# Optimization experiments

Hardware: AMD Instinct MI355X
Metric: run time of the kernel (lower is better)

The kernel has to match this reference:

```python
import jax, jax.numpy as jnp
import numpy as np

B, T1, S = 32, 129, 256
E, H, K, V, VOCAB = 512, 1024, 128, 128, 8000


def _lstm_cell(x, h, c, W_ih, W_hh, b):
    # PyTorch LSTMCell gate order: i, f, g, o
    gates = x @ W_ih.T + h @ W_hh.T + b  # [B, 4H]
    i, f, g, o = jnp.split(gates, 4, axis=-1)
    c_new = jax.nn.sigmoid(f) * c + jax.nn.sigmoid(i) * jnp.tanh(g)
    h_new = jax.nn.sigmoid(o) * jnp.tanh(c_new)
    return h_new, c_new


def setup_inputs() -> dict:
    key = jax.random.key(0)
    ks = jax.random.split(key, 16)
    w = lambda k, shp: (jax.random.normal(k, shp, dtype=jnp.float32) * 0.02)
    return {
        "decoder_inputs": jax.random.randint(ks[0], (B, T1), 0, VOCAB),
        "inputs_lens": jax.random.randint(ks[1], (B,), 0, T1 - 1),
        "encoder_hidden": jax.random.normal(ks[2], (B, H), dtype=jnp.float32),
        "encoder_keys": jax.random.normal(ks[3], (B, S, K), dtype=jnp.float32),
        "encoder_values": jax.random.normal(ks[4], (B, S, V), dtype=jnp.float32),
        "embedding": w(ks[5], (VOCAB, E)),
        "W_ih1": w(ks[6], (4 * H, E + V)),
        "W_hh1": w(ks[7], (4 * H, H)),
        "b1": jnp.zeros((4 * H,), dtype=jnp.float32),
        "W_ih2": w(ks[8], (4 * H, H)),
        "W_hh2": w(ks[9], (4 * H, H)),
        "b2": jnp.zeros((4 * H,), dtype=jnp.float32),
        "W_q": w(ks[10], (K, H)),
        "b_q": jnp.zeros((K,), dtype=jnp.float32),
        "W_out": w(ks[11], (VOCAB, H + V)),
        "b_out": jnp.zeros((VOCAB,), dtype=jnp.float32),
    }


def reference(decoder_inputs, inputs_lens, encoder_hidden, encoder_keys,
              encoder_values, embedding, W_ih1, W_hh1, b1, W_ih2, W_hh2, b2,
              W_q, b_q, W_out, b_out):
    T = decoder_inputs.shape[1] - 1  # max_len = inputs.size(1) - 1
    # Teacher-forced embeddings, gathered once: [T, B, E]
    emb = jnp.swapaxes(embedding[decoder_inputs[:, :T]], 0, 1)

    h1 = h2 = encoder_hidden
    c1 = c2 = jnp.zeros_like(encoder_hidden)
    context0 = jnp.zeros((encoder_hidden.shape[0], encoder_values.shape[-1]),
                         dtype=encoder_hidden.dtype)

    def step(carry, emb_t):
        h1, c1, h2, c2, context = carry
        x = jnp.concatenate([emb_t, context], axis=1)  # [B, E+V]
        h1, c1 = _lstm_cell(x, h1, c1, W_ih1, W_hh1, b1)
        h2, c2 = _lstm_cell(h1, h2, c2, W_ih2, W_hh2, b2)
        # Attention over encoder keys/values
        q = h2 @ W_q.T + b_q                               # [B, K]
        energy = jnp.einsum('bsk,bk->bs', encoder_keys, q)  # [B, S]
        attn = jax.nn.softmax(energy, axis=-1)
        context = jnp.einsum('bs,bsv->bv', attn, encoder_values)  # [B, V]
        logits = jnp.concatenate([h2, context], axis=1) @ W_out.T + b_out
        return (h1, c1, h2, c2, context), logits

    _, logits = jax.lax.scan(step, (h1, c1, h2, c2, context0), emb)
    return jnp.swapaxes(logits, 0, 1)  # [B, T, VOCAB]
```

## Files before the change

kernel.cpp:

```cpp
#include <hip/hip_runtime.h>
#include <hip/hip_bf16.h>
#include <cstddef>

#define BB    32
#define T1    129
#define TT    128
#define SS    256
#define EE    512
#define HH    1024
#define KK    128
#define VV    128
#define VOC   8000
#define VOCP  8064
#define K1    1664
#define K2    2048
#define KLOG  1152
#define NF1   13
#define NF2   16
#define NBLK  256
#define NATT  32

typedef __bf16 bf16x8 __attribute__((ext_vector_type(8)));
typedef float  f32x4  __attribute__((ext_vector_type(4)));

#define MFMA(a,b,c) __builtin_amdgcn_mfma_f32_16x16x32_bf16((a),(b),(c),0,0,0)

#define CLOAD(dst, p) asm volatile("global_load_dwordx4 %0, %1, off sc0 sc1" : "=v"(dst) : "v"(p))

__device__ __forceinline__ int coh_load_i32(const int* p) {
    int r;
    asm volatile("global_load_dword %0, %1, off sc0 sc1\n\ts_waitcnt vmcnt(0)"
                 : "=v"(r) : "v"(p) : "memory");
    return r;
}
__device__ __forceinline__ void cstore_u16(__hip_bfloat16* p, __hip_bfloat16 v) {
    union { __hip_bfloat16 h; unsigned short u; } cv; cv.h = v;
    unsigned int val = cv.u;
    asm volatile("global_store_short %0, %1, off sc0 sc1" :: "v"(p), "v"(val) : "memory");
}
__device__ __forceinline__ void cstore_f32(float* p, float v) {
    asm volatile("global_store_dword %0, %1, off sc0 sc1" :: "v"(p), "v"(v) : "memory");
}

union bf8u { __hip_bfloat16 h[8]; bf16x8 v; };

__device__ __forceinline__ bf16x8 cvt8(float4 a, float4 b) {
    bf8u u;
    u.h[0] = __float2bfloat16(a.x); u.h[1] = __float2bfloat16(a.y);
    u.h[2] = __float2bfloat16(a.z); u.h[3] = __float2bfloat16(a.w);
    u.h[4] = __float2bfloat16(b.x); u.h[5] = __float2bfloat16(b.y);
    u.h[6] = __float2bfloat16(b.z); u.h[7] = __float2bfloat16(b.w);
    return u.v;
}

template<int SBASE, int NS>
__device__ __forceinline__ void coh_mfma(const __hip_bfloat16* rA, const __hip_bfloat16* rB,
                                         int wv, const bf16x8* wf, f32x4& a0, f32x4& a1)
{
    bf16x8 fA[NS], fB[NS];
    #pragma unroll
    for (int s = 0; s < NS; ++s) {
        int k0 = (wv + 4 * (SBASE + s)) * 32;
        CLOAD(fA[s], rA + k0);
        CLOAD(fB[s], rB + k0);
    }
    asm volatile("s_waitcnt vmcnt(0)" ::: "memory");
    __builtin_amdgcn_sched_barrier(0);
    #pragma unroll
    for (int s = 0; s < NS; ++s) {
        a0 = MFMA(fA[s], wf[SBASE + s], a0);
        a1 = MFMA(fB[s], wf[SBASE + s], a1);
    }
}

__device__ __forceinline__ void grid_barrier(int* bar, int bid, int& gen)
{
    asm volatile("s_waitcnt vmcnt(0)" ::: "memory");
    __syncthreads();
    if (threadIdx.x == 0) {
        int target = gen + 1;
        int prev = __hip_atomic_fetch_add(&bar[(bid >> 5) * 32], 1,
                                          __ATOMIC_RELAXED, __HIP_MEMORY_SCOPE_AGENT);
        if (((prev + 1) & 31) == 0) {
            int pr = __hip_atomic_fetch_add(&bar[320], 1,
                                            __ATOMIC_RELAXED, __HIP_MEMORY_SCOPE_AGENT);
            if (((pr + 1) & 7) == 0)
                __hip_atomic_fetch_add(&bar[384], 1,
                                       __ATOMIC_RELAXED, __HIP_MEMORY_SCOPE_AGENT);
        }
        while (coh_load_i32(&bar[384]) < target)
            __builtin_amdgcn_s_sleep(4);
        gen = target;
    }
    __syncthreads();
}

__global__ void pack_wout(const float* __restrict__ W, __hip_bfloat16* __restrict__ Wp)
{
    int v = blockIdx.y;
    int k = blockIdx.x * 256 + threadIdx.x;
    if (k >= KLOG) return;
    float w = (v < VOC) ? W[(size_t)v * KLOG + k] : 0.f;
    Wp[(size_t)v * KLOG + k] = __float2bfloat16(w);
}

__global__ void init_state(const float* __restrict__ enc,
                           __hip_bfloat16* __restrict__ A1,
                           __hip_bfloat16* __restrict__ A2,
                           int* __restrict__ bar)
{
    int i = blockIdx.x * 256 + threadIdx.x;
    if (i < 1024) bar[i] = 0;
    if (i >= BB * HH) return;
    int b = i >> 10, j = i & 1023;
    float e = enc[i];
    __hip_bfloat16 eb = __float2bfloat16(e);
    A2[(size_t)b * K2 + HH + j]        = eb;
    A1[(size_t)b * K1 + (EE + VV) + j] = eb;
    if (j < VV) A1[(size_t)b * K1 + EE + j] = __float2bfloat16(0.f);
}

__global__ void gather_emb(const int* __restrict__ tok, const float* __restrict__ emb,
                           __hip_bfloat16* __restrict__ A1)
{
    int bid = blockIdx.x;
    int t = bid >> 5, b = bid & 31;
    int id = tok[b * T1 + t];
    const float* er = emb + (size_t)id * EE;
    __hip_bfloat16* dst = A1 + (size_t)t * BB * K1 + (size_t)b * K1;
    for (int k = threadIdx.x; k < EE; k += 256)
        dst[k] = __float2bfloat16(er[k]);
}

__global__ __launch_bounds__(256) void decoder_persistent(
    const float* __restrict__ Wih1, const float* __restrict__ Whh1, const float* __restrict__ b1v,
    const float* __restrict__ Wih2, const float* __restrict__ Whh2, const float* __restrict__ b2v,
    const float* __restrict__ Wq,   const float* __restrict__ bq,
    const float* __restrict__ keys, const float* __restrict__ vals,
    __hip_bfloat16* A1, __hip_bfloat16* A2,
    __hip_bfloat16* Alog, float* h2f, int* bar)
{
    const int bid = blockIdx.x;
    const int tid = threadIdx.x;
    const int wv  = tid >> 6;
    const int l   = tid & 63;
    const int l15 = l & 15, l4 = l >> 4;
    const int n0  = bid * 16;

    __shared__ float G[4][32][17];
    __shared__ float hs[HH];
    __shared__ float qs[KK];
    __shared__ float es[SS];
    __shared__ float red[256];

    bf16x8 w1f[NF1], w2f[NF2];
    {
        const int col  = n0 + l15;
        const int orow = (col & 3) * HH + (col >> 2);
        #pragma unroll
        for (int s = 0; s < NF1; ++s) {
            int k0 = (wv + 4 * s) * 32 + l4 * 8;
            const float* src = (k0 < EE + VV) ? (Wih1 + (size_t)orow * (EE + VV) + k0)
                                              : (Whh1 + (size_t)orow * HH + (k0 - (EE + VV)));
            w1f[s] = cvt8(*(const float4*)src, *(const float4*)(src + 4));
        }
        #pragma unroll
        for (int s = 0; s < NF2; ++s) {
            int k0 = (wv + 4 * s) * 32 + l4 * 8;
            const float* src = (k0 < HH) ? (Wih2 + (size_t)orow * HH + k0)
                                         : (Whh2 + (size_t)orow * HH + (k0 - HH));
            w2f[s] = cvt8(*(const float4*)src, *(const float4*)(src + 4));
        }
    }

    float c1r = 0.f, c2r = 0.f;
    float gb1[4], gb2[4];
    {
        int jl = (tid >> 5) & 3;
        int j  = (n0 >> 2) + jl;
        #pragma unroll
        for (int g = 0; g < 4; ++g) { gb1[g] = b1v[g * HH + j]; gb2[g] = b2v[g * HH + j]; }
    }

    int gen = 0;
    const size_t a1s = (size_t)BB * K1;
    const size_t a2s = (size_t)BB * K2;

    #pragma unroll 1
    for (int t = 0; t < TT; ++t) {
        const __hip_bfloat16* A1t = A1 + (size_t)t * a1s;
        __hip_bfloat16* A1n   = A1 + (size_t)(t + 1) * a1s;
        __hip_bfloat16* A2c   = A2 + (size_t)(t & 1) * a2s;
        __hip_bfloat16* A2n   = A2 + (size_t)((t + 1) & 1) * a2s;
        __hip_bfloat16* AlogT = Alog + (size_t)t * BB * KLOG;

        {
            f32x4 acc0 = {0.f,0.f,0.f,0.f}, acc1 = {0.f,0.f,0.f,0.f};
            const __hip_bfloat16* rA = A1t + (size_t)l15 * K1 + l4 * 8;
            const __hip_bfloat16* rB = rA + (size_t)16 * K1;
            #pragma unroll
            for (int s = 0; s < 4; ++s) {
                int k0 = (wv + 4 * s) * 32;
                bf16x8 a0 = *(const bf16x8*)(rA + k0);
                bf16x8 a1 = *(const bf16x8*)(rB + k0);
                acc0 = MFMA(a0, w1f[s], acc0);
                acc1 = MFMA(a1, w1f[s], acc1);
            }
            coh_mfma<4, 9>(rA, rB, wv, w1f, acc0, acc1);

            #pragma unroll
            for (int r = 0; r < 4; ++r) {
                G[wv][l4 * 4 + r][l15]      = acc0[r];
                G[wv][16 + l4 * 4 + r][l15] = acc1[r];
            }
        }
        __syncthreads();
        if (tid < 128) {
            int b = tid & 31, jl = tid >> 5;
            float g0 = G[0][b][4*jl+0] + G[1][b][4*jl+0] + G[2][b][4*jl+0] + G[3][b][4*jl+0] + gb1[0];
            float g1 = G[0][b][4*jl+1] + G[1][b][4*jl+1] + G[2][b][4*jl+1] + G[3][b][4*jl+1] + gb1[1];
            float g2 = G[0][b][4*jl+2] + G[1][b][4*jl+2] + G[2][b][4*jl+2] + G[3][b][4*jl+2] + gb1[2];
            float g3 = G[0][b][4*jl+3] + G[1][b][4*jl+3] + G[2][b][4*jl+3] + G[3][b][4*jl+3] + gb1[3];
            float si = 1.f / (1.f + __expf(-g0));
            float sf = 1.f / (1.f + __expf(-g1));
            float so = 1.f / (1.f + __expf(-g3));
            c1r = sf * c1r + si * tanhf(g2);
            float h = so * tanhf(c1r);
            int j = (n0 >> 2) + jl;
            __hip_bfloat16 hb = __float2bfloat16(h);
            cstore_u16(&A2c[(size_t)b * K2 + j], hb);
            if (t + 1 < TT) cstore_u16(&A1n[(size_t)b * K1 + EE + VV + j], hb);
        }
        grid_barrier(bar, bid, gen);

        {
            f32x4 acc0 = {0.f,0.f,0.f,0.f}, acc1 = {0.f,0.f,0.f,0.f};
            const __hip_bfloat16* rA = A2c + (size_t)l15 * K2 + l4 * 8;
            const __hip_bfloat16* rB = rA + (size_t)16 * K2;
            coh_mfma<0, 8>(rA, rB, wv, w2f, acc0, acc1);
            coh_mfma<8, 8>(rA, rB, wv, w2f, acc0, acc1);
            #pragma unroll
            for (int r = 0; r < 4; ++r) {
                G[wv][l4 * 4 + r][l15]      = acc0[r];
                G[wv][16 + l4 * 4 + r][l15] = acc1[r];
            }
        }
        __syncthreads();
        if (tid < 128) {
            int b = tid & 31, jl = tid >> 5;
            float g0 = G[0][b][4*jl+0] + G[1][b][4*jl+0] + G[2][b][4*jl+0] + G[3][b][4*jl+0] + gb2[0];
            float g1 = G[0][b][4*jl+1] + G[1][b][4*jl+1] + G[2][b][4*jl+1] + G[3][b][4*jl+1] + gb2[1];
            float g2 = G[0][b][4*jl+2] + G[1][b][4*jl+2] + G[2][b][4*jl+2] + G[3][b][4*jl+2] + gb2[2];
            float g3 = G[0][b][4*jl+3] + G[1][b][4*jl+3] + G[2][b][4*jl+3] + G[3][b][4*jl+3] + gb2[3];
            float si = 1.f / (1.f + __expf(-g0));
            float sf = 1.f / (1.f + __expf(-g1));
            float so = 1.f / (1.f + __expf(-g3));
            c2r = sf * c2r + si * tanhf(g2);
            float h = so * tanhf(c2r);
            int j = (n0 >> 2) + jl;
            __hip_bfloat16 hb = __float2bfloat16(h);
            cstore_u16(&A2n[(size_t)b * K2 + HH + j], hb);
            AlogT[(size_t)b * KLOG + j] = hb;
            cstore_f32(&h2f[b * HH + j], h);
        }
        grid_barrier(bar, bid, gen);

        if (bid < NATT) {
            const int b = bid;
            {
                float4 hv;
                const float* hp = h2f + (size_t)b * HH + tid * 4;
                CLOAD(hv, hp);
                asm volatile("s_waitcnt vmcnt(0)" ::: "memory");
                __builtin_amdgcn_sched_barrier(0);
                *(float4*)&hs[tid * 4] = hv;
            }
            __syncthreads();
            {
                int k = tid & 127, hf = tid >> 7;
                const float* wr = Wq + (size_t)k * HH + hf * 512;
                const float* hh = hs + hf * 512;
                float acc = 0.f;
                for (int j2 = 0; j2 < 512; j2 += 4)
                    acc += wr[j2]*hh[j2] + wr[j2+1]*hh[j2+1] + wr[j2+2]*hh[j2+2] + wr[j2+3]*hh[j2+3];
                red[tid] = acc;
            }
            __syncthreads();
            if (tid < KK) qs[tid] = red[tid] + red[tid + 128] + bq[tid];
            __syncthreads();
            {
                int s = tid;
                const float4* kr = (const float4*)(keys + ((size_t)b * SS + s) * KK);
                float acc = 0.f;
                for (int k4 = 0; k4 < KK / 4; ++k4) {
                    float4 kv = kr[k4];
                    acc += kv.x*qs[k4*4] + kv.y*qs[k4*4+1] + kv.z*qs[k4*4+2] + kv.w*qs[k4*4+3];
                }
                es[s] = acc;
            }
            __syncthreads();
            red[tid] = es[tid];
            __syncthreads();
            for (int off = 128; off > 0; off >>= 1) {
                if (tid < off) red[tid] = fmaxf(red[tid], red[tid + off]);
                __syncthreads();
            }
            float mx = red[0];
            __syncthreads();
            float ev = __expf(es[tid] - mx);
            es[tid] = ev; red[tid] = ev;
            __syncthreads();
            for (int off = 128; off > 0; off >>= 1) {
                if (tid < off) red[tid] += red[tid + off];
                __syncthreads();
            }
            float inv = 1.f / red[0];
            __syncthreads();
            {
                int v = tid & 127, hf = tid >> 7;
                const float* vb = vals + ((size_t)b * SS + hf * 128) * VV;
                float acc = 0.f;
                for (int s = 0; s < 128; ++s) acc += es[hf * 128 + s] * vb[(size_t)s * VV + v];
                red[tid] = acc;
            }
            __syncthreads();
            if (tid < VV) {
                float cv = (red[tid] + red[tid + 128]) * inv;
                __hip_bfloat16 cb = __float2bfloat16(cv);
                if (t + 1 < TT) cstore_u16(&A1n[(size_t)b * K1 + EE + tid], cb);
                AlogT[(size_t)b * KLOG + HH + tid] = cb;
            }
        }
        grid_barrier(bar, bid, gen);
    }
}

__global__ __launch_bounds__(256) void logits_gemm(
    const __hip_bfloat16* __restrict__ Alog,
    const __hip_bfloat16* __restrict__ W,
    const float* __restrict__ bout,
    float* __restrict__ out)
{
    int n0 = blockIdx.x * 128;
    int m0 = blockIdx.y * 128;
    int wv = threadIdx.x >> 6, l = threadIdx.x & 63;
    int l15 = l & 15, l4 = l >> 4;

    f32x4 acc[8][2] = {};
    const __hip_bfloat16* Ap = Alog + (size_t)(m0 + l15) * KLOG + l4 * 8;
    const __hip_bfloat16* Bp = W    + (size_t)(n0 + wv * 32 + l15) * KLOG + l4 * 8;

    for (int kt = 0; kt < KLOG; kt += 32) {
        bf16x8 b0 = *(const bf16x8*)(Bp + kt);
        bf16x8 b1 = *(const bf16x8*)(Bp + (size_t)16 * KLOG + kt);
        #pragma unroll
        for (int ms = 0; ms < 8; ++ms) {
            bf16x8 a = *(const bf16x8*)(Ap + (size_t)ms * 16 * KLOG + kt);
            acc[ms][0] = MFMA(a, b0, acc[ms][0]);
            acc[ms][1] = MFMA(a, b1, acc[ms][1]);
        }
    }

    #pragma unroll
    for (int ms = 0; ms < 8; ++ms) {
        #pragma unroll
        for (int ns = 0; ns < 2; ++ns) {
            int col = n0 + wv * 32 + ns * 16 + l15;
            if (col < VOC) {
                float bias = bout[col];
                #pragma unroll
                for (int r = 0; r < 4; ++r) {
                    int m = m0 + ms * 16 + l4 * 4 + r;
                    int b = m & 31, t = m >> 5;
                    out[((size_t)b * TT + t) * VOC + col] = acc[ms][ns][r] + bias;
                }
            }
        }
    }
}

extern "C" void kernel_launch(void* const* d_in, const int* in_sizes, int n_in,
                              void* d_out, int out_size, void* d_ws, size_t ws_size,
                              hipStream_t stream)
{
    (void)in_sizes; (void)n_in; (void)out_size; (void)ws_size;
    const int*   dec  = (const int*)  d_in[0];
    const float* enc  = (const float*)d_in[2];
    const float* keys = (const float*)d_in[3];
    const float* vals = (const float*)d_in[4];
    const float* emb  = (const float*)d_in[5];
    const float* Wih1 = (const float*)d_in[6];
    const float* Whh1 = (const float*)d_in[7];
    const float* b1   = (const float*)d_in[8];
    const float* Wih2 = (const float*)d_in[9];
    const float* Whh2 = (const float*)d_in[10];
    const float* b2   = (const float*)d_in[11];
    const float* Wq   = (const float*)d_in[12];
    const float* bq   = (const float*)d_in[13];
    const float* Wout = (const float*)d_in[14];
    const float* bout = (const float*)d_in[15];
    float* out = (float*)d_out;

    char* p = (char*)d_ws;
    __hip_bfloat16* WoutP = (__hip_bfloat16*)p; p += (size_t)VOCP * KLOG * 2;
    __hip_bfloat16* A1    = (__hip_bfloat16*)p; p += (size_t)TT * BB * K1 * 2;
    __hip_bfloat16* A2    = (__hip_bfloat16*)p; p += (size_t)2 * BB * K2 * 2;
    __hip_bfloat16* Alog  = (__hip_bfloat16*)p; p += (size_t)TT * BB * KLOG * 2;
    float* h2f = (float*)p; p += (size_t)BB * HH * 4;
    int*   bar = (int*)p;   p += 4096;

    pack_wout  <<<dim3((KLOG + 255) / 256, VOCP), 256, 0, stream>>>(Wout, WoutP);
    init_state <<<dim3(128), 256, 0, stream>>>(enc, A1, A2, bar);
    gather_emb <<<dim3(TT * BB), 256, 0, stream>>>(dec, emb, A1);

    decoder_persistent<<<dim3(NBLK), 256, 0, stream>>>(
        Wih1, Whh1, b1, Wih2, Whh2, b2, Wq, bq, keys, vals,
        A1, A2, Alog, h2f, bar);

    logits_gemm<<<dim3(VOCP / 128, (BB * TT) / 128), 256, 0, stream>>>(Alog, WoutP, bout, out);
}
```

Baseline: 5.061 ms.

## Precompute embedding gates, overlap hidden-state GEMMs, halve persistent grid

```diff
diff --git a/kernel.cpp b/kernel.cpp
--- a/kernel.cpp
+++ b/kernel.cpp
@@ -12,34 +12,32 @@
 #define VV    128
 #define VOC   8000
 #define VOCP  8064
-#define K1    1664
-#define K2    2048
 #define KLOG  1152
-#define NF1   13
-#define NF2   16
-#define NBLK  256
+#define NB2   128
 #define NATT  32
 
 typedef __bf16 bf16x8 __attribute__((ext_vector_type(8)));
 typedef float  f32x4  __attribute__((ext_vector_type(4)));
+typedef unsigned int u32x4 __attribute__((ext_vector_type(4)));
 
 #define MFMA(a,b,c) __builtin_amdgcn_mfma_f32_16x16x32_bf16((a),(b),(c),0,0,0)
-
-#define CLOAD(dst, p) asm volatile("global_load_dwordx4 %0, %1, off sc0 sc1" : "=v"(dst) : "v"(p))
-
+#define VMCNT0 do { asm volatile("s_waitcnt vmcnt(0)" ::: "memory"); \
+                    __builtin_amdgcn_sched_barrier(0); } while (0)
+
+__device__ __forceinline__ void cload_b8(bf16x8& d, const __hip_bfloat16* p) {
+    asm volatile("global_load_dwordx4 %0, %1, off sc0 sc1" : "=v"(d) : "v"(p));
+}
+__device__ __forceinline__ void cload_f4(f32x4& d, const float* p) {
+    asm volatile("global_load_dwordx4 %0, %1, off sc0 sc1" : "=v"(d) : "v"(p));
+}
 __device__ __forceinline__ int coh_load_i32(const int* p) {
     int r;
     asm volatile("global_load_dword %0, %1, off sc0 sc1\n\ts_waitcnt vmcnt(0)"
                  : "=v"(r) : "v"(p) : "memory");
     return r;
 }
-__device__ __forceinline__ void cstore_u16(__hip_bfloat16* p, __hip_bfloat16 v) {
-    union { __hip_bfloat16 h; unsigned short u; } cv; cv.h = v;
-    unsigned int val = cv.u;
-    asm volatile("global_store_short %0, %1, off sc0 sc1" :: "v"(p), "v"(val) : "memory");
-}
-__device__ __forceinline__ void cstore_f32(float* p, float v) {
-    asm volatile("global_store_dword %0, %1, off sc0 sc1" :: "v"(p), "v"(v) : "memory");
+__device__ __forceinline__ void cstore16(const void* p, u32x4 v) {
+    asm volatile("global_store_dwordx4 %0, %1, off sc0 sc1" :: "v"(p), "v"(v) : "memory");
 }
 
 union bf8u { __hip_bfloat16 h[8]; bf16x8 v; };
@@ -52,26 +50,10 @@
     u.h[6] = __float2bfloat16(b.z); u.h[7] = __float2bfloat16(b.w);
     return u.v;
 }
-
-template<int SBASE, int NS>
-__device__ __forceinline__ void coh_mfma(const __hip_bfloat16* rA, const __hip_bfloat16* rB,
-                                         int wv, const bf16x8* wf, f32x4& a0, f32x4& a1)
-{
-    bf16x8 fA[NS], fB[NS];
-    #pragma unroll
-    for (int s = 0; s < NS; ++s) {
-        int k0 = (wv + 4 * (SBASE + s)) * 32;
-        CLOAD(fA[s], rA + k0);
-        CLOAD(fB[s], rB + k0);
-    }
-    asm volatile("s_waitcnt vmcnt(0)" ::: "memory");
-    __builtin_amdgcn_sched_barrier(0);
-    #pragma unroll
-    for (int s = 0; s < NS; ++s) {
-        a0 = MFMA(fA[s], wf[SBASE + s], a0);
-        a1 = MFMA(fB[s], wf[SBASE + s], a1);
-    }
-}
+__device__ __forceinline__ float bfu(unsigned short u) {
+    return __uint_as_float(((unsigned)u) << 16);
+}
+__device__ __forceinline__ float fsig(float x)  { return 1.f / (1.f + __expf(-x)); }
 
 __device__ __forceinline__ void grid_barrier(int* bar, int bid, int& gen)
 {
@@ -79,17 +61,17 @@
     __syncthreads();
     if (threadIdx.x == 0) {
         int target = gen + 1;
-        int prev = __hip_atomic_fetch_add(&bar[(bid >> 5) * 32], 1,
+        int prev = __hip_atomic_fetch_add(&bar[(bid >> 3) * 32], 1,
                                           __ATOMIC_RELAXED, __HIP_MEMORY_SCOPE_AGENT);
-        if (((prev + 1) & 31) == 0) {
-            int pr = __hip_atomic_fetch_add(&bar[320], 1,
+        if (((prev + 1) & 7) == 0) {
+            int pr = __hip_atomic_fetch_add(&bar[640], 1,
                                             __ATOMIC_RELAXED, __HIP_MEMORY_SCOPE_AGENT);
-            if (((pr + 1) & 7) == 0)
-                __hip_atomic_fetch_add(&bar[384], 1,
+            if (((pr + 1) & 15) == 0)
+                __hip_atomic_fetch_add(&bar[768], 1,
                                        __ATOMIC_RELAXED, __HIP_MEMORY_SCOPE_AGENT);
         }
-        while (coh_load_i32(&bar[384]) < target)
-            __builtin_amdgcn_s_sleep(4);
+        while (coh_load_i32(&bar[768]) < target)
+            __builtin_amdgcn_s_sleep(2);
         gen = target;
     }
     __syncthreads();
@@ -104,202 +86,288 @@
     Wp[(size_t)v * KLOG + k] = __float2bfloat16(w);
 }
 
+__global__ void pack_w1emb(const float* __restrict__ Wih1, __hip_bfloat16* __restrict__ Wp)
+{
+    int rp = blockIdx.y;
+    int k  = blockIdx.x * 256 + threadIdx.x;
+    if (k >= EE) return;
+    int orow = (rp & 3) * HH + (rp >> 2);
+    Wp[(size_t)rp * EE + k] = __float2bfloat16(Wih1[(size_t)orow * (EE + VV) + k]);
+}
+
 __global__ void init_state(const float* __restrict__ enc,
-                           __hip_bfloat16* __restrict__ A1,
-                           __hip_bfloat16* __restrict__ A2,
+                           __hip_bfloat16* __restrict__ H1,
+                           __hip_bfloat16* __restrict__ H2,
+                           __hip_bfloat16* __restrict__ CTX,
                            int* __restrict__ bar)
 {
     int i = blockIdx.x * 256 + threadIdx.x;
     if (i < 1024) bar[i] = 0;
+    if (i < BB * VV) CTX[i] = __float2bfloat16(0.f);
     if (i >= BB * HH) return;
-    int b = i >> 10, j = i & 1023;
-    float e = enc[i];
-    __hip_bfloat16 eb = __float2bfloat16(e);
-    A2[(size_t)b * K2 + HH + j]        = eb;
-    A1[(size_t)b * K1 + (EE + VV) + j] = eb;
-    if (j < VV) A1[(size_t)b * K1 + EE + j] = __float2bfloat16(0.f);
+    __hip_bfloat16 eb = __float2bfloat16(enc[i]);
+    H1[i] = eb;
+    H2[i] = eb;
 }
 
 __global__ void gather_emb(const int* __restrict__ tok, const float* __restrict__ emb,
-                           __hip_bfloat16* __restrict__ A1)
+                           __hip_bfloat16* __restrict__ Aemb)
 {
     int bid = blockIdx.x;
     int t = bid >> 5, b = bid & 31;
     int id = tok[b * T1 + t];
     const float* er = emb + (size_t)id * EE;
-    __hip_bfloat16* dst = A1 + (size_t)t * BB * K1 + (size_t)b * K1;
+    __hip_bfloat16* dst = Aemb + (size_t)bid * EE;
     for (int k = threadIdx.x; k < EE; k += 256)
         dst[k] = __float2bfloat16(er[k]);
 }
 
-__global__ __launch_bounds__(256) void decoder_persistent(
+__global__ __launch_bounds__(256) void g1emb_gemm(
+    const __hip_bfloat16* __restrict__ A,
+    const __hip_bfloat16* __restrict__ W,
+    __hip_bfloat16* __restrict__ C)
+{
+    int n0 = blockIdx.x * 128;
+    int m0 = blockIdx.y * 128;
+    int wv = threadIdx.x >> 6, l = threadIdx.x & 63;
+    int l15 = l & 15, l4 = l >> 4;
+
+    f32x4 acc[8][2] = {};
+    const __hip_bfloat16* Ap = A + (size_t)(m0 + l15) * EE + l4 * 8;
+    const __hip_bfloat16* Bp = W + (size_t)(n0 + wv * 32 + l15) * EE + l4 * 8;
+
+    for (int kt = 0; kt < EE; kt += 32) {
+        bf16x8 b0 = *(const bf16x8*)(Bp + kt);
+        bf16x8 b1 = *(const bf16x8*)(Bp + (size_t)16 * EE + kt);
+        #pragma unroll
+        for (int ms = 0; ms < 8; ++ms) {
+            bf16x8 a = *(const bf16x8*)(Ap + (size_t)ms * 16 * EE + kt);
+            acc[ms][0] = MFMA(a, b0, acc[ms][0]);
+            acc[ms][1] = MFMA(a, b1, acc[ms][1]);
+        }
+    }
+    #pragma unroll
+    for (int ms = 0; ms < 8; ++ms)
+        #pragma unroll
+        for (int ns = 0; ns < 2; ++ns) {
+            int col = n0 + wv * 32 + ns * 16 + l15;
+            #pragma unroll
+            for (int r = 0; r < 4; ++r) {
+                int m = m0 + ms * 16 + l4 * 4 + r;
+                C[(size_t)m * 4096 + col] = __float2bfloat16(acc[ms][ns][r]);
+            }
+        }
+}
+
+__global__ __launch_bounds__(512, 2) void decoder_persistent(
     const float* __restrict__ Wih1, const float* __restrict__ Whh1, const float* __restrict__ b1v,
     const float* __restrict__ Wih2, const float* __restrict__ Whh2, const float* __restrict__ b2v,
     const float* __restrict__ Wq,   const float* __restrict__ bq,
     const float* __restrict__ keys, const float* __restrict__ vals,
-    __hip_bfloat16* A1, __hip_bfloat16* A2,
-    __hip_bfloat16* Alog, float* h2f, int* bar)
+    const __hip_bfloat16* __restrict__ G1,
+    __hip_bfloat16* H1, __hip_bfloat16* H2, __hip_bfloat16* CTX,
+    float* h2f, __hip_bfloat16* Alog, int* bar)
 {
     const int bid = blockIdx.x;
     const int tid = threadIdx.x;
-    const int wv  = tid >> 6;
+    const int w   = tid >> 6;
+    const int cg  = w >> 2;
+    const int kq  = w & 3;
     const int l   = tid & 63;
     const int l15 = l & 15, l4 = l >> 4;
-    const int n0  = bid * 16;
-
-    __shared__ float G[4][32][17];
-    __shared__ float hs[HH];
+    const int n0  = bid * 32 + cg * 16;
+
+    __shared__ float G[2][4][32][17];
+    __shared__ alignas(16) __hip_bfloat16 hstage[32][8];
+    __shared__ alignas(16) float hstagef[32][8];
+    __shared__ alignas(16) __hip_bfloat16 cstage[128];
+    __shared__ alignas(16) float hs[HH];
     __shared__ float qs[KK];
     __shared__ float es[SS];
-    __shared__ float red[256];
-
-    bf16x8 w1f[NF1], w2f[NF2];
+    __shared__ float red[512];
+
+    bf16x8 w1c, w1h[8], w2a[8], w2b[8];
     {
         const int col  = n0 + l15;
         const int orow = (col & 3) * HH + (col >> 2);
-        #pragma unroll
-        for (int s = 0; s < NF1; ++s) {
-            int k0 = (wv + 4 * s) * 32 + l4 * 8;
-            const float* src = (k0 < EE + VV) ? (Wih1 + (size_t)orow * (EE + VV) + k0)
-                                              : (Whh1 + (size_t)orow * HH + (k0 - (EE + VV)));
-            w1f[s] = cvt8(*(const float4*)src, *(const float4*)(src + 4));
-        }
-        #pragma unroll
-        for (int s = 0; s < NF2; ++s) {
-            int k0 = (wv + 4 * s) * 32 + l4 * 8;
-            const float* src = (k0 < HH) ? (Wih2 + (size_t)orow * HH + k0)
-                                         : (Whh2 + (size_t)orow * HH + (k0 - HH));
-            w2f[s] = cvt8(*(const float4*)src, *(const float4*)(src + 4));
+        {
+            int k0 = kq * 32 + l4 * 8;
+            const float* s = Wih1 + (size_t)orow * (EE + VV) + EE + k0;
+            w1c = cvt8(*(const float4*)s, *(const float4*)(s + 4));
+        }
+        #pragma unroll
+        for (int s = 0; s < 8; ++s) {
+            int k0 = kq * 256 + s * 32 + l4 * 8;
+            const float* p1 = Whh1 + (size_t)orow * HH + k0;
+            const float* p2 = Wih2 + (size_t)orow * HH + k0;
+            const float* p3 = Whh2 + (size_t)orow * HH + k0;
+            w1h[s] = cvt8(*(const float4*)p1, *(const float4*)(p1 + 4));
+            w2a[s] = cvt8(*(const float4*)p2, *(const float4*)(p2 + 4));
+            w2b[s] = cvt8(*(const float4*)p3, *(const float4*)(p3 + 4));
         }
     }
 
     float c1r = 0.f, c2r = 0.f;
     float gb1[4], gb2[4];
     {
-        int jl = (tid >> 5) & 3;
-        int j  = (n0 >> 2) + jl;
+        int jl = tid & 7;
+        int j  = bid * 8 + jl;
         #pragma unroll
         for (int g = 0; g < 4; ++g) { gb1[g] = b1v[g * HH + j]; gb2[g] = b2v[g * HH + j]; }
     }
 
+    f32x4 acc1A = {0,0,0,0}, acc1B = {0,0,0,0}, acc2A = {0,0,0,0}, acc2B = {0,0,0,0};
+    #pragma unroll
+    for (int s = 0; s < 8; ++s) {
+        int k0 = kq * 256 + s * 32 + l4 * 8;
+        bf16x8 a0 = *(const bf16x8*)(H1 + (size_t)l15 * HH + k0);
+        bf16x8 a1 = *(const bf16x8*)(H1 + (size_t)(16 + l15) * HH + k0);
+        acc1A = MFMA(a0, w1h[s], acc1A);
+        acc1B = MFMA(a1, w1h[s], acc1B);
+        bf16x8 b0 = *(const bf16x8*)(H2 + (size_t)l15 * HH + k0);
+        bf16x8 b1 = *(const bf16x8*)(H2 + (size_t)(16 + l15) * HH + k0);
+        acc2A = MFMA(b0, w2b[s], acc2A);
+        acc2B = MFMA(b1, w2b[s], acc2B);
+    }
+
     int gen = 0;
-    const size_t a1s = (size_t)BB * K1;
-    const size_t a2s = (size_t)BB * K2;
+    grid_barrier(bar, bid, gen);
+
+    bf16x8 fA[8], fB[8];
 
     #pragma unroll 1
     for (int t = 0; t < TT; ++t) {
-        const __hip_bfloat16* A1t = A1 + (size_t)t * a1s;
-        __hip_bfloat16* A1n   = A1 + (size_t)(t + 1) * a1s;
-        __hip_bfloat16* A2c   = A2 + (size_t)(t & 1) * a2s;
-        __hip_bfloat16* A2n   = A2 + (size_t)((t + 1) & 1) * a2s;
         __hip_bfloat16* AlogT = Alog + (size_t)t * BB * KLOG;
 
-        {
-            f32x4 acc0 = {0.f,0.f,0.f,0.f}, acc1 = {0.f,0.f,0.f,0.f};
-            const __hip_bfloat16* rA = A1t + (size_t)l15 * K1 + l4 * 8;
-            const __hip_bfloat16* rB = rA + (size_t)16 * K1;
-            #pragma unroll
-            for (int s = 0; s < 4; ++s) {
-                int k0 = (wv + 4 * s) * 32;
-                bf16x8 a0 = *(const bf16x8*)(rA + k0);
-                bf16x8 a1 = *(const bf16x8*)(rB + k0);
-                acc0 = MFMA(a0, w1f[s], acc0);
-                acc1 = MFMA(a1, w1f[s], acc1);
-            }
-            coh_mfma<4, 9>(rA, rB, wv, w1f, acc0, acc1);
-
-            #pragma unroll
-            for (int r = 0; r < 4; ++r) {
-                G[wv][l4 * 4 + r][l15]      = acc0[r];
-                G[wv][16 + l4 * 4 + r][l15] = acc1[r];
-            }
-        }
+        if (t > 0) {
+            int k0 = kq * 32 + l4 * 8;
+            cload_b8(fA[0], CTX + (size_t)l15 * VV + k0);
+            cload_b8(fB[0], CTX + (size_t)(16 + l15) * VV + k0);
+            VMCNT0;
+            acc1A = MFMA(fA[0], w1c, acc1A);
+            acc1B = MFMA(fB[0], w1c, acc1B);
+        }
+        #pragma unroll
+        for (int r = 0; r < 4; ++r) {
+            G[cg][kq][l4 * 4 + r][l15]      = acc1A[r];
+            G[cg][kq][16 + l4 * 4 + r][l15] = acc1B[r];
+        }
+        acc1A = (f32x4){0,0,0,0}; acc1B = (f32x4){0,0,0,0};
         __syncthreads();
-        if (tid < 128) {
-            int b = tid & 31, jl = tid >> 5;
-            float g0 = G[0][b][4*jl+0] + G[1][b][4*jl+0] + G[2][b][4*jl+0] + G[3][b][4*jl+0] + gb1[0];
-            float g1 = G[0][b][4*jl+1] + G[1][b][4*jl+1] + G[2][b][4*jl+1] + G[3][b][4*jl+1] + gb1[1];
-            float g2 = G[0][b][4*jl+2] + G[1][b][4*jl+2] + G[2][b][4*jl+2] + G[3][b][4*jl+2] + gb1[2];
-            float g3 = G[0][b][4*jl+3] + G[1][b][4*jl+3] + G[2][b][4*jl+3] + G[3][b][4*jl+3] + gb1[3];
-            float si = 1.f / (1.f + __expf(-g0));
-            float sf = 1.f / (1.f + __expf(-g1));
-            float so = 1.f / (1.f + __expf(-g3));
-            c1r = sf * c1r + si * tanhf(g2);
-            float h = so * tanhf(c1r);
-            int j = (n0 >> 2) + jl;
-            __hip_bfloat16 hb = __float2bfloat16(h);
-            cstore_u16(&A2c[(size_t)b * K2 + j], hb);
-            if (t + 1 < TT) cstore_u16(&A1n[(size_t)b * K1 + EE + VV + j], hb);
-        }
+        if (tid < 256) {
+            int b = tid >> 3, jl = tid & 7;
+            int cg2 = jl >> 2, cb = (jl & 3) * 4;
+            const __hip_bfloat16* gp = G1 + ((size_t)(t * 32 + b)) * 4096 + bid * 32 + jl * 4;
+            ushort4 gu = *(const ushort4*)gp;
+            float g0 = G[cg2][0][b][cb+0] + G[cg2][1][b][cb+0] + G[cg2][2][b][cb+0] + G[cg2][3][b][cb+0] + bfu(gu.x) + gb1[0];
+            float g1 = G[cg2][0][b][cb+1] + G[cg2][1][b][cb+1] + G[cg2][2][b][cb+1] + G[cg2][3][b][cb+1] + bfu(gu.y) + gb1[1];
+            float g2 = G[cg2][0][b][cb+2] + G[cg2][1][b][cb+2] + G[cg2][2][b][cb+2] + G[cg2][3][b][cb+2] + bfu(gu.z) + gb1[2];
+            float g3 = G[cg2][0][b][cb+3] + G[cg2][1][b][cb+3] + G[cg2][2][b][cb+3] + G[cg2][3][b][cb+3] + bfu(gu.w) + gb1[3];
+            c1r = fsig(g1) * c1r + fsig(g0) * tanhf(g2);
+            float h = fsig(g3) * tanhf(c1r);
+            hstage[b][jl] = __float2bfloat16(h);
+        }
+        __syncthreads();
+        if (tid < 32)
+            cstore16(H1 + (size_t)tid * HH + bid * 8, *(const u32x4*)&hstage[tid][0]);
         grid_barrier(bar, bid, gen);
 
-        {
-            f32x4 acc0 = {0.f,0.f,0.f,0.f}, acc1 = {0.f,0.f,0.f,0.f};
-            const __hip_bfloat16* rA = A2c + (size_t)l15 * K2 + l4 * 8;
-            const __hip_bfloat16* rB = rA + (size_t)16 * K2;
-            coh_mfma<0, 8>(rA, rB, wv, w2f, acc0, acc1);
-            coh_mfma<8, 8>(rA, rB, wv, w2f, acc0, acc1);
-            #pragma unroll
-            for (int r = 0; r < 4; ++r) {
-                G[wv][l4 * 4 + r][l15]      = acc0[r];
-                G[wv][16 + l4 * 4 + r][l15] = acc1[r];
-            }
-        }
+        #pragma unroll
+        for (int s = 0; s < 8; ++s) {
+            int k0 = kq * 256 + s * 32 + l4 * 8;
+            cload_b8(fA[s], H1 + (size_t)l15 * HH + k0);
+            cload_b8(fB[s], H1 + (size_t)(16 + l15) * HH + k0);
+        }
+        VMCNT0;
+        #pragma unroll
+        for (int s = 0; s < 8; ++s) {
+            acc2A = MFMA(fA[s], w2a[s], acc2A);
+            acc2B = MFMA(fB[s], w2a[s], acc2B);
+            acc1A = MFMA(fA[s], w1h[s], acc1A);
+            acc1B = MFMA(fB[s], w1h[s], acc1B);
+        }
+        #pragma unroll
+        for (int r = 0; r < 4; ++r) {
+            G[cg][kq][l4 * 4 + r][l15]      = acc2A[r];
+            G[cg][kq][16 + l4 * 4 + r][l15] = acc2B[r];
+        }
+        acc2A = (f32x4){0,0,0,0}; acc2B = (f32x4){0,0,0,0};
         __syncthreads();
-        if (tid < 128) {
-            int b = tid & 31, jl = tid >> 5;
-            float g0 = G[0][b][4*jl+0] + G[1][b][4*jl+0] + G[2][b][4*jl+0] + G[3][b][4*jl+0] + gb2[0];
-            float g1 = G[0][b][4*jl+1] + G[1][b][4*jl+1] + G[2][b][4*jl+1] + G[3][b][4*jl+1] + gb2[1];
-            float g2 = G[0][b][4*jl+2] + G[1][b][4*jl+2] + G[2][b][4*jl+2] + G[3][b][4*jl+2] + gb2[2];
-            float g3 = G[0][b][4*jl+3] + G[1][b][4*jl+3] + G[2][b][4*jl+3] + G[3][b][4*jl+3] + gb2[3];
-            float si = 1.f / (1.f + __expf(-g0));
-            float sf = 1.f / (1.f + __expf(-g1));
-            float so = 1.f / (1.f + __expf(-g3));
-            c2r = sf * c2r + si * tanhf(g2);
-            float h = so * tanhf(c2r);
-            int j = (n0 >> 2) + jl;
-            __hip_bfloat16 hb = __float2bfloat16(h);
-            cstore_u16(&A2n[(size_t)b * K2 + HH + j], hb);
-            AlogT[(size_t)b * KLOG + j] = hb;
-            cstore_f32(&h2f[b * HH + j], h);
+        if (tid < 256) {
+            int b = tid >> 3, jl = tid & 7;
+            int cg2 = jl >> 2, cb = (jl & 3) * 4;
+            float g0 = G[cg2][0][b][cb+0] + G[cg2][1][b][cb+0] + G[cg2][2][b][cb+0] + G[cg2][3][b][cb+0] + gb2[0];
+            float g1 = G[cg2][0][b][cb+1] + G[cg2][1][b][cb+1] + G[cg2][2][b][cb+1] + G[cg2][3][b][cb+1] + gb2[1];
+            float g2 = G[cg2][0][b][cb+2] + G[cg2][1][b][cb+2] + G[cg2][2][b][cb+2] + G[cg2][3][b][cb+2] + gb2[2];
+            float g3 = G[cg2][0][b][cb+3] + G[cg2][1][b][cb+3] + G[cg2][2][b][cb+3] + G[cg2][3][b][cb+3] + gb2[3];
+            c2r = fsig(g1) * c2r + fsig(g0) * tanhf(g2);
+            float h = fsig(g3) * tanhf(c2r);
+            hstage[b][jl]  = __float2bfloat16(h);
+            hstagef[b][jl] = h;
+        }
+        __syncthreads();
+        if (tid < 32) {
+            u32x4 v = *(const u32x4*)&hstage[tid][0];
+            cstore16(H2 + (size_t)tid * HH + bid * 8, v);
+            *(u32x4*)(AlogT + (size_t)tid * KLOG + bid * 8) = v;
+            cstore16(h2f + (size_t)tid * HH + bid * 8,     *(const u32x4*)&hstagef[tid][0]);
+            cstore16(h2f + (size_t)tid * HH + bid * 8 + 4, *(const u32x4*)&hstagef[tid][4]);
         }
         grid_barrier(bar, bid, gen);
+
+        #pragma unroll
+        for (int s = 0; s < 8; ++s) {
+            int k0 = kq * 256 + s * 32 + l4 * 8;
+            cload_b8(fA[s], H2 + (size_t)l15 * HH + k0);
+            cload_b8(fB[s], H2 + (size_t)(16 + l15) * HH + k0);
+        }
+        VMCNT0;
+        #pragma unroll
+        for (int s = 0; s < 8; ++s) {
+            acc2A = MFMA(fA[s], w2b[s], acc2A);
+            acc2B = MFMA(fB[s], w2b[s], acc2B);
+        }
 
         if (bid < NATT) {
             const int b = bid;
+            if (tid < 256) {
+                f32x4 hv;
+                cload_f4(hv, h2f + (size_t)b * HH + tid * 4);
+                VMCNT0;
+                *(f32x4*)&hs[tid * 4] = hv;
+            }
+            __syncthreads();
             {
-                float4 hv;
-                const float* hp = h2f + (size_t)b * HH + tid * 4;
-                CLOAD(hv, hp);
-                asm volatile("s_waitcnt vmcnt(0)" ::: "memory");
-                __builtin_amdgcn_sched_barrier(0);
-                *(float4*)&hs[tid * 4] = hv;
-            }
+                int kp = tid >> 2, qc = tid & 3;
+                const float4* wr = (const float4*)(Wq + (size_t)kp * HH + qc * 256);
+                const float* hh = hs + qc * 256;
+                float acc = 0.f;
+                #pragma unroll 4
+                for (int c = 0; c < 64; ++c) {
+                    float4 wv4 = wr[c];
+                    acc += wv4.x*hh[c*4] + wv4.y*hh[c*4+1] + wv4.z*hh[c*4+2] + wv4.w*hh[c*4+3];
+                }
+                red[tid] = acc;
+            }
+            __syncthreads();
+            if (tid < KK) qs[tid] = red[tid*4] + red[tid*4+1] + red[tid*4+2] + red[tid*4+3] + bq[tid];
             __syncthreads();
             {
-                int k = tid & 127, hf = tid >> 7;
-                const float* wr = Wq + (size_t)k * HH + hf * 512;
-                const float* hh = hs + hf * 512;
+                int s = tid >> 1, hf = tid & 1;
+                const float4* kr = (const float4*)(keys + ((size_t)b * SS + s) * KK + hf * 64);
+                const float* qh = qs + hf * 64;
                 float acc = 0.f;
-                for (int j2 = 0; j2 < 512; j2 += 4)
-                    acc += wr[j2]*hh[j2] + wr[j2+1]*hh[j2+1] + wr[j2+2]*hh[j2+2] + wr[j2+3]*hh[j2+3];
+                #pragma unroll
+                for (int k4 = 0; k4 < 16; ++k4) {
+                    float4 kv = kr[k4];
+                    acc += kv.x*qh[k4*4] + kv.y*qh[k4*4+1] + kv.z*qh[k4*4+2] + kv.w*qh[k4*4+3];
+                }
                 red[tid] = acc;
             }
             __syncthreads();
-            if (tid < KK) qs[tid] = red[tid] + red[tid + 128] + bq[tid];
-            __syncthreads();
-            {
-                int s = tid;
-                const float4* kr = (const float4*)(keys + ((size_t)b * SS + s) * KK);
-                float acc = 0.f;
-                for (int k4 = 0; k4 < KK / 4; ++k4) {
-                    float4 kv = kr[k4];
-                    acc += kv.x*qs[k4*4] + kv.y*qs[k4*4+1] + kv.z*qs[k4*4+2] + kv.w*qs[k4*4+3];
-                }
-                es[s] = acc;
-            }
-            __syncthreads();
-            red[tid] = es[tid];
+            if (tid < SS) es[tid] = red[tid*2] + red[tid*2+1];
+            __syncthreads();
+            if (tid < SS) red[tid] = es[tid];
             __syncthreads();
             for (int off = 128; off > 0; off >>= 1) {
                 if (tid < off) red[tid] = fmaxf(red[tid], red[tid + off]);
@@ -307,8 +375,7 @@
             }
             float mx = red[0];
             __syncthreads();
-            float ev = __expf(es[tid] - mx);
-            es[tid] = ev; red[tid] = ev;
+            if (tid < SS) { float ev = __expf(es[tid] - mx); es[tid] = ev; red[tid] = ev; }
             __syncthreads();
             for (int off = 128; off > 0; off >>= 1) {
                 if (tid < off) red[tid] += red[tid + off];
@@ -317,18 +384,22 @@
             float inv = 1.f / red[0];
             __syncthreads();
             {
-                int v = tid & 127, hf = tid >> 7;
-                const float* vb = vals + ((size_t)b * SS + hf * 128) * VV;
+                int v = tid & 127, sh = tid >> 7;
+                const float* vb = vals + ((size_t)b * SS + sh * 64) * VV + v;
                 float acc = 0.f;
-                for (int s = 0; s < 128; ++s) acc += es[hf * 128 + s] * vb[(size_t)s * VV + v];
+                for (int i = 0; i < 64; ++i) acc += es[sh * 64 + i] * vb[(size_t)i * VV];
                 red[tid] = acc;
             }
             __syncthreads();
             if (tid < VV) {
-                float cv = (red[tid] + red[tid + 128]) * inv;
-                __hip_bfloat16 cb = __float2bfloat16(cv);
-                if (t + 1 < TT) cstore_u16(&A1n[(size_t)b * K1 + EE + tid], cb);
-                AlogT[(size_t)b * KLOG + HH + tid] = cb;
+                float cv = (red[tid] + red[tid+128] + red[tid+256] + red[tid+384]) * inv;
+                cstage[tid] = __float2bfloat16(cv);
+            }
+            __syncthreads();
+            if (tid < 16) {
+                u32x4 v = *(const u32x4*)&cstage[tid * 8];
+                cstore16(CTX + (size_t)b * VV + tid * 8, v);
+                *(u32x4*)(AlogT + (size_t)b * KLOG + HH + tid * 8) = v;
             }
         }
         grid_barrier(bar, bid, gen);
@@ -360,9 +431,8 @@
             acc[ms][1] = MFMA(a, b1, acc[ms][1]);
         }
     }
-
     #pragma unroll
-    for (int ms = 0; ms < 8; ++ms) {
+    for (int ms = 0; ms < 8; ++ms)
         #pragma unroll
         for (int ns = 0; ns < 2; ++ns) {
             int col = n0 + wv * 32 + ns * 16 + l15;
@@ -376,7 +446,6 @@
                 }
             }
         }
-    }
 }
 
 extern "C" void kernel_launch(void* const* d_in, const int* in_sizes, int n_in,
@@ -403,19 +472,25 @@
 
     char* p = (char*)d_ws;
     __hip_bfloat16* WoutP = (__hip_bfloat16*)p; p += (size_t)VOCP * KLOG * 2;
-    __hip_bfloat16* A1    = (__hip_bfloat16*)p; p += (size_t)TT * BB * K1 * 2;
-    __hip_bfloat16* A2    = (__hip_bfloat16*)p; p += (size_t)2 * BB * K2 * 2;
+    __hip_bfloat16* G1    = (__hip_bfloat16*)p; p += (size_t)TT * BB * 4 * HH * 2;
     __hip_bfloat16* Alog  = (__hip_bfloat16*)p; p += (size_t)TT * BB * KLOG * 2;
+    __hip_bfloat16* H1    = (__hip_bfloat16*)p; p += (size_t)BB * HH * 2;
+    __hip_bfloat16* H2    = (__hip_bfloat16*)p; p += (size_t)BB * HH * 2;
+    __hip_bfloat16* CTX   = (__hip_bfloat16*)p; p += (size_t)BB * VV * 2;
     float* h2f = (float*)p; p += (size_t)BB * HH * 4;
-    int*   bar = (int*)p;   p += 4096;
+    int* bar = (int*)p; p += 4096;
+    __hip_bfloat16* Aemb  = Alog;
+    __hip_bfloat16* Wp1e  = Alog + (size_t)TT * BB * EE;
 
     pack_wout  <<<dim3((KLOG + 255) / 256, VOCP), 256, 0, stream>>>(Wout, WoutP);
-    init_state <<<dim3(128), 256, 0, stream>>>(enc, A1, A2, bar);
-    gather_emb <<<dim3(TT * BB), 256, 0, stream>>>(dec, emb, A1);
-
-    decoder_persistent<<<dim3(NBLK), 256, 0, stream>>>(
+    pack_w1emb <<<dim3(2, 4 * HH), 256, 0, stream>>>(Wih1, Wp1e);
+    init_state <<<dim3(128), 256, 0, stream>>>(enc, H1, H2, CTX, bar);
+    gather_emb <<<dim3(TT * BB), 256, 0, stream>>>(dec, emb, Aemb);
+    g1emb_gemm <<<dim3(32, 32), 256, 0, stream>>>(Aemb, Wp1e, G1);
+
+    decoder_persistent<<<dim3(NB2), 512, 0, stream>>>(
         Wih1, Whh1, b1, Wih2, Whh2, b2, Wq, bq, keys, vals,
-        A1, A2, Alog, h2f, bar);
+        G1, H1, H2, CTX, h2f, Alog, bar);
 
     logits_gemm<<<dim3(VOCP / 128, (BB * TT) / 128), 256, 0, stream>>>(Alog, WoutP, bout, out);
 }
```

Measured after the change: 9.065 ms. 1.79x slower.
